# Optimization experiments

Measured on AMD Instinct MI355X. Metric: run time of the kernel, lower is better.

The kernel has to match this reference:

```python
import jax, jax.numpy as jnp
import numpy as np

N_NODES = 10000
N_EDGES = 160000
D = 256
P = 2.0  # exponent in |h_i - h_j|**p


def setup_inputs() -> dict:
    key = jax.random.key(0)
    k1, k2, k3, k4 = jax.random.split(key, 4)
    X = jax.random.normal(k1, (N_NODES, D), dtype=jnp.float32)
    edge_index = jax.random.randint(k2, (2, N_EDGES), 0, N_NODES, dtype=jnp.int64)
    # SAGEConv parameters (scaled like Glorot init)
    scale = 1.0 / np.sqrt(D)
    W_root = jax.random.normal(k3, (D, D), dtype=jnp.float32) * scale
    W_neigh = jax.random.normal(k4, (D, D), dtype=jnp.float32) * scale
    b = jnp.zeros((D,), dtype=jnp.float32)
    return {"X": X, "edge_index": edge_index, "W_root": W_root,
            "W_neigh": W_neigh, "b": b}


def reference(X, edge_index, W_root, W_neigh, b):
    n = X.shape[0]
    row, col = edge_index[0], edge_index[1]
    # degree of each target (row) node, used for both SAGE mean and scatter-mean
    ones = jnp.ones((row.shape[0],), dtype=X.dtype)
    deg = jax.ops.segment_sum(ones, row, num_segments=n)           # [N]
    denom = jnp.maximum(deg, 1.0)[:, None]                         # avoid 0-div
    # SAGEConv: h_i = W_root x_i + W_neigh mean_{j in N(i)} x_j + b
    neigh_sum = jax.ops.segment_sum(X[col], row, num_segments=n)   # [N, D]
    neigh_mean = neigh_sum / denom
    H = jax.nn.relu(X @ W_root + neigh_mean @ W_neigh + b)         # [N, D]
    # gather node diffs -> pow -> scatter-mean by row -> tanh
    diffs = jnp.abs(H[row] - H[col]) ** P                          # [E, D]
    gg = jax.ops.segment_sum(diffs, row, num_segments=n) / denom   # [N, D]
    return jnp.tanh(gg)
```

## Files before the change

### kernel.cpp

```cpp
#include <hip/hip_runtime.h>
#include <math.h>

#define N_NODES 10000
#define N_EDGES 160000
#define D 256
#define KDIM 512
#define CAP 64
#define SPLIT 5000

typedef short bf16x8 __attribute__((ext_vector_type(8)));
typedef float f32x4 __attribute__((ext_vector_type(4)));
typedef unsigned short u16x4 __attribute__((ext_vector_type(4)));
typedef unsigned short ushort_t;

__device__ __forceinline__ ushort_t f2bf(float f) {
    unsigned u = __builtin_bit_cast(unsigned, f);
    unsigned r = (u + 0x7fffu + ((u >> 16) & 1u)) >> 16;
    return (ushort_t)r;
}
__device__ __forceinline__ float bf2f(ushort_t u) {
    unsigned v = ((unsigned)u) << 16;
    return __builtin_bit_cast(float, v);
}

#define ZERO_BLOCKS 79
#define PREPW_BLOCKS 128
#define CASTX_BLOCKS 2500

__global__ void k_init(int* __restrict__ cursors,
                       const float* __restrict__ Wr, const float* __restrict__ Wn,
                       ushort_t* __restrict__ Wb,
                       const float* __restrict__ X, ushort_t* __restrict__ A) {
    __shared__ float tile[32][33];
    int b = blockIdx.x;
    int t = threadIdx.x;
    if (b < ZERO_BLOCKS) {
        int i = b * 256 + t;
        if (i < 2 * N_NODES) cursors[i] = 0;
    } else if (b < ZERO_BLOCKS + PREPW_BLOCKS) {
        int wb = b - ZERO_BLOCKS;
        int k0 = (wb & 15) * 32, n0 = (wb >> 4) * 32;
        {
            int r = t >> 3, c4 = t & 7;
            int k = k0 + r;
            const float* src = (k < D) ? (Wr + (size_t)k * D + n0 + c4 * 4)
                                       : (Wn + (size_t)(k - D) * D + n0 + c4 * 4);
            float4 v = *(const float4*)src;
            tile[r][c4 * 4 + 0] = v.x; tile[r][c4 * 4 + 1] = v.y;
            tile[r][c4 * 4 + 2] = v.z; tile[r][c4 * 4 + 3] = v.w;
        }
        __syncthreads();
        {
            int n = t >> 3, kq = t & 7;
            ushort4 o = make_ushort4(f2bf(tile[kq * 4 + 0][n]), f2bf(tile[kq * 4 + 1][n]),
                                     f2bf(tile[kq * 4 + 2][n]), f2bf(tile[kq * 4 + 3][n]));
            *(ushort4*)(Wb + (size_t)(n0 + n) * KDIM + k0 + kq * 4) = o;
        }
    } else {
        int nb = b - ZERO_BLOCKS - PREPW_BLOCKS;
        int node = nb * 4 + (t >> 6), lane = t & 63;
        if (node < N_NODES) {
            float4 v = *(const float4*)(X + (size_t)node * D + lane * 4);
            ushort4 o = make_ushort4(f2bf(v.x), f2bf(v.y), f2bf(v.z), f2bf(v.w));
            *(ushort4*)(A + (size_t)node * KDIM + lane * 4) = o;
        }
    }
}

__global__ void k_fill(const int* __restrict__ row, const int* __restrict__ col,
                       int* __restrict__ curLo, int* __restrict__ curHi,
                       int* __restrict__ csr_col, int e) {
    int i = blockIdx.x * blockDim.x + threadIdx.x;
    if (i < e) {
        int r = row[i], c = col[i];
        if (c < SPLIT) {
            int p = atomicAdd(&curLo[r], 1);
            csr_col[r * CAP + p] = c;
        } else {
            int p = atomicAdd(&curHi[r], 1);
            csr_col[r * CAP + CAP - 1 - p] = c;
        }
    }
}

__global__ void k_mean(const int* __restrict__ curLo, const int* __restrict__ curHi,
                       const int* __restrict__ csr_col, ushort_t* __restrict__ A) {
    int node = blockIdx.x * 4 + (threadIdx.x >> 6);
    int lane = threadIdx.x & 63;
    if (node >= N_NODES) return;
    int s0 = node * CAP;
    int nlo = curLo[node], nhi = curHi[node];
    float ax = 0.f, ay = 0.f, az = 0.f, aw = 0.f;
    #pragma unroll 1
    for (int half = 0; half < 2; ++half) {
        int s = half ? (s0 + CAP - nhi) : s0;
        int t = half ? (s0 + CAP) : (s0 + nlo);
        int e = s;
        for (; e + 8 <= t; e += 8) {
            int j0 = csr_col[e + 0], j1 = csr_col[e + 1], j2 = csr_col[e + 2], j3 = csr_col[e + 3];
            int j4 = csr_col[e + 4], j5 = csr_col[e + 5], j6 = csr_col[e + 6], j7 = csr_col[e + 7];
            ushort4 v0 = *(const ushort4*)(A + (size_t)j0 * KDIM + lane * 4);
            ushort4 v1 = *(const ushort4*)(A + (size_t)j1 * KDIM + lane * 4);
            ushort4 v2 = *(const ushort4*)(A + (size_t)j2 * KDIM + lane * 4);
            ushort4 v3 = *(const ushort4*)(A + (size_t)j3 * KDIM + lane * 4);
            ushort4 v4 = *(const ushort4*)(A + (size_t)j4 * KDIM + lane * 4);
            ushort4 v5 = *(const ushort4*)(A + (size_t)j5 * KDIM + lane * 4);
            ushort4 v6 = *(const ushort4*)(A + (size_t)j6 * KDIM + lane * 4);
            ushort4 v7 = *(const ushort4*)(A + (size_t)j7 * KDIM + lane * 4);
            ax += bf2f(v0.x) + bf2f(v1.x) + bf2f(v2.x) + bf2f(v3.x)
                + bf2f(v4.x) + bf2f(v5.x) + bf2f(v6.x) + bf2f(v7.x);
            ay += bf2f(v0.y) + bf2f(v1.y) + bf2f(v2.y) + bf2f(v3.y)
                + bf2f(v4.y) + bf2f(v5.y) + bf2f(v6.y) + bf2f(v7.y);
            az += bf2f(v0.z) + bf2f(v1.z) + bf2f(v2.z) + bf2f(v3.z)
                + bf2f(v4.z) + bf2f(v5.z) + bf2f(v6.z) + bf2f(v7.z);
            aw += bf2f(v0.w) + bf2f(v1.w) + bf2f(v2.w) + bf2f(v3.w)
                + bf2f(v4.w) + bf2f(v5.w) + bf2f(v6.w) + bf2f(v7.w);
        }
        for (; e < t; ++e) {
            int j = csr_col[e];
            ushort4 v = *(const ushort4*)(A + (size_t)j * KDIM + lane * 4);
            ax += bf2f(v.x); ay += bf2f(v.y); az += bf2f(v.z); aw += bf2f(v.w);
        }
    }
    int deg = nlo + nhi;
    float inv = 1.f / (float)(deg > 1 ? deg : 1);
    u16x4 o;
    o[0] = f2bf(ax * inv); o[1] = f2bf(ay * inv);
    o[2] = f2bf(az * inv); o[3] = f2bf(aw * inv);
    __builtin_nontemporal_store(o, (u16x4*)(A + (size_t)node * KDIM + D + lane * 4));
}

#define BM 64
#define BN 128
#define BK 32
#define LDK 40

__global__ __launch_bounds__(256) void k_gemm(
    const ushort_t* __restrict__ A, const ushort_t* __restrict__ Wb,
    const float* __restrict__ bias, ushort_t* __restrict__ H) {
    __shared__ ushort_t As[BM][LDK];
    __shared__ ushort_t Bs[BN][LDK];

    int tid = threadIdx.x;
    int lane = tid & 63;
    int wave = tid >> 6;
    int wm = wave >> 1;
    int wn = wave & 1;
    int row0 = blockIdx.x * BM;
    int col0 = blockIdx.y * BN;

    f32x4 acc[2][4];
    #pragma unroll
    for (int i = 0; i < 2; ++i)
        #pragma unroll
        for (int j = 0; j < 4; ++j)
            acc[i][j] = (f32x4){0.f, 0.f, 0.f, 0.f};

    int r_a = tid >> 2;
    int kq = tid & 3;

    for (int kk = 0; kk < KDIM; kk += BK) {
        int ga = row0 + r_a; if (ga >= N_NODES) ga = N_NODES - 1;
        ushort4 a0 = *(const ushort4*)(A + (size_t)ga * KDIM + kk + kq * 8);
        ushort4 a1 = *(const ushort4*)(A + (size_t)ga * KDIM + kk + kq * 8 + 4);
        ushort4 b0 = *(const ushort4*)(Wb + (size_t)(col0 + r_a) * KDIM + kk + kq * 8);
        ushort4 b1 = *(const ushort4*)(Wb + (size_t)(col0 + r_a) * KDIM + kk + kq * 8 + 4);
        ushort4 b2 = *(const ushort4*)(Wb + (size_t)(col0 + r_a + 64) * KDIM + kk + kq * 8);
        ushort4 b3 = *(const ushort4*)(Wb + (size_t)(col0 + r_a + 64) * KDIM + kk + kq * 8 + 4);

        __syncthreads();
        *(ushort4*)&As[r_a][kq * 8]          = a0;
        *(ushort4*)&As[r_a][kq * 8 + 4]      = a1;
        *(ushort4*)&Bs[r_a][kq * 8]          = b0;
        *(ushort4*)&Bs[r_a][kq * 8 + 4]      = b1;
        *(ushort4*)&Bs[r_a + 64][kq * 8]     = b2;
        *(ushort4*)&Bs[r_a + 64][kq * 8 + 4] = b3;
        __syncthreads();

        int fr = lane & 15, fg = (lane >> 4) * 8;
        bf16x8 aF[2], bF[4];
        #pragma unroll
        for (int mf = 0; mf < 2; ++mf)
            aF[mf] = *(const bf16x8*)&As[wm * 32 + mf * 16 + fr][fg];
        #pragma unroll
        for (int nf = 0; nf < 4; ++nf)
            bF[nf] = *(const bf16x8*)&Bs[wn * 64 + nf * 16 + fr][fg];
        #pragma unroll
        for (int mf = 0; mf < 2; ++mf)
            #pragma unroll
            for (int nf = 0; nf < 4; ++nf)
                acc[mf][nf] = __builtin_amdgcn_mfma_f32_16x16x32_bf16(
                    aF[mf], bF[nf], acc[mf][nf], 0, 0, 0);
    }

    int fc = lane & 15, frow = (lane >> 4) * 4;
    #pragma unroll
    for (int nf = 0; nf < 4; ++nf) {
        int c = col0 + wn * 64 + nf * 16 + fc;
        float bc = bias[c];
        #pragma unroll
        for (int mf = 0; mf < 2; ++mf) {
            #pragma unroll
            for (int q = 0; q < 4; ++q) {
                int r = row0 + wm * 32 + mf * 16 + frow + q;
                if (r < N_NODES) {
                    float h = acc[mf][nf][q] + bc;
                    H[(size_t)r * D + c] = f2bf(h > 0.f ? h : 0.f);
                }
            }
        }
    }
}

__global__ void k_out(const ushort_t* __restrict__ H,
                      const int* __restrict__ curLo, const int* __restrict__ curHi,
                      const int* __restrict__ csr_col,
                      float* __restrict__ out) {
    int node = blockIdx.x * 4 + (threadIdx.x >> 6);
    int lane = threadIdx.x & 63;
    if (node >= N_NODES) return;
    ushort4 hb = *(const ushort4*)(H + (size_t)node * D + lane * 4);
    float hx = bf2f(hb.x), hy = bf2f(hb.y), hz = bf2f(hb.z), hw = bf2f(hb.w);
    int s0 = node * CAP;
    int nlo = curLo[node], nhi = curHi[node];
    float ax = 0.f, ay = 0.f, az = 0.f, aw = 0.f;
    #pragma unroll 1
    for (int half = 0; half < 2; ++half) {
        int s = half ? (s0 + CAP - nhi) : s0;
        int t = half ? (s0 + CAP) : (s0 + nlo);
        int e = s;
        for (; e + 8 <= t; e += 8) {
            int j0 = csr_col[e + 0], j1 = csr_col[e + 1], j2 = csr_col[e + 2], j3 = csr_col[e + 3];
            int j4 = csr_col[e + 4], j5 = csr_col[e + 5], j6 = csr_col[e + 6], j7 = csr_col[e + 7];
            ushort4 v0 = *(const ushort4*)(H + (size_t)j0 * D + lane * 4);
            ushort4 v1 = *(const ushort4*)(H + (size_t)j1 * D + lane * 4);
            ushort4 v2 = *(const ushort4*)(H + (size_t)j2 * D + lane * 4);
            ushort4 v3 = *(const ushort4*)(H + (size_t)j3 * D + lane * 4);
            ushort4 v4 = *(const ushort4*)(H + (size_t)j4 * D + lane * 4);
            ushort4 v5 = *(const ushort4*)(H + (size_t)j5 * D + lane * 4);
            ushort4 v6 = *(const ushort4*)(H + (size_t)j6 * D + lane * 4);
            ushort4 v7 = *(const ushort4*)(H + (size_t)j7 * D + lane * 4);
            float d;
            d = hx - bf2f(v0.x); ax += d * d;  d = hy - bf2f(v0.y); ay += d * d;
            d = hz - bf2f(v0.z); az += d * d;  d = hw - bf2f(v0.w); aw += d * d;
            d = hx - bf2f(v1.x); ax += d * d;  d = hy - bf2f(v1.y); ay += d * d;
            d = hz - bf2f(v1.z); az += d * d;  d = hw - bf2f(v1.w); aw += d * d;
            d = hx - bf2f(v2.x); ax += d * d;  d = hy - bf2f(v2.y); ay += d * d;
            d = hz - bf2f(v2.z); az += d * d;  d = hw - bf2f(v2.w); aw += d * d;
            d = hx - bf2f(v3.x); ax += d * d;  d = hy - bf2f(v3.y); ay += d * d;
            d = hz - bf2f(v3.z); az += d * d;  d = hw - bf2f(v3.w); aw += d * d;
            d = hx - bf2f(v4.x); ax += d * d;  d = hy - bf2f(v4.y); ay += d * d;
            d = hz - bf2f(v4.z); az += d * d;  d = hw - bf2f(v4.w); aw += d * d;
            d = hx - bf2f(v5.x); ax += d * d;  d = hy - bf2f(v5.y); ay += d * d;
            d = hz - bf2f(v5.z); az += d * d;  d = hw - bf2f(v5.w); aw += d * d;
            d = hx - bf2f(v6.x); ax += d * d;  d = hy - bf2f(v6.y); ay += d * d;
            d = hz - bf2f(v6.z); az += d * d;  d = hw - bf2f(v6.w); aw += d * d;
            d = hx - bf2f(v7.x); ax += d * d;  d = hy - bf2f(v7.y); ay += d * d;
            d = hz - bf2f(v7.z); az += d * d;  d = hw - bf2f(v7.w); aw += d * d;
        }
        for (; e < t; ++e) {
            int j = csr_col[e];
            ushort4 v = *(const ushort4*)(H + (size_t)j * D + lane * 4);
            float d;
            d = hx - bf2f(v.x); ax += d * d;  d = hy - bf2f(v.y); ay += d * d;
            d = hz - bf2f(v.z); az += d * d;  d = hw - bf2f(v.w); aw += d * d;
        }
    }
    int deg = nlo + nhi;
    float inv = 1.f / (float)(deg > 1 ? deg : 1);
    f32x4 o;
    o[0] = tanhf(ax * inv); o[1] = tanhf(ay * inv);
    o[2] = tanhf(az * inv); o[3] = tanhf(aw * inv);
    __builtin_nontemporal_store(o, (f32x4*)(out + (size_t)node * D + lane * 4));
}


extern "C" void kernel_launch(void* const* d_in, const int* in_sizes, int n_in,
                              void* d_out, int out_size, void* d_ws, size_t ws_size,
                              hipStream_t stream) {
    const float* X    = (const float*)d_in[0];
    const int*   edge = (const int*)d_in[1];
    const float* Wr   = (const float*)d_in[2];
    const float* Wn   = (const float*)d_in[3];
    const float* bias = (const float*)d_in[4];
    float* out = (float*)d_out;

    char* ws = (char*)d_ws;
    size_t off = 0;
    auto alloc = [&](size_t bytes) -> void* {
        void* p = ws + off;
        off += (bytes + 255) & ~(size_t)255;
        return p;
    };
    int*      cursors = (int*)alloc(sizeof(int) * 2 * N_NODES);
    int*      csr_col = (int*)alloc(sizeof(int) * N_NODES * CAP);
    ushort_t* A       = (ushort_t*)alloc(sizeof(ushort_t) * (size_t)N_NODES * KDIM);
    ushort_t* Wb      = (ushort_t*)alloc(sizeof(ushort_t) * (size_t)D * KDIM);
    ushort_t* H       = (ushort_t*)alloc(sizeof(ushort_t) * (size_t)N_NODES * D);

    int* curLo = cursors;
    int* curHi = cursors + N_NODES;
    const int* row = edge;
    const int* col = edge + N_EDGES;

    k_init<<<ZERO_BLOCKS + PREPW_BLOCKS + CASTX_BLOCKS, 256, 0, stream>>>(
        cursors, Wr, Wn, Wb, X, A);
    k_fill<<<(N_EDGES + 255) / 256, 256, 0, stream>>>(row, col, curLo, curHi,
                                                      csr_col, N_EDGES);
    k_mean<<<2500, 256, 0, stream>>>(curLo, curHi, csr_col, A);

    dim3 ggrid((N_NODES + BM - 1) / BM, D / BN);
    k_gemm<<<ggrid, 256, 0, stream>>>(A, Wb, bias, H);

    k_out<<<2500, 256, 0, stream>>>(H, curLo, curHi, csr_col, out);
}
```

Measured before the change: 67.58 us.

## Split feature dimension into halves so gathers fit in cache

The gather kernels (mean aggregation and the output diff-pow-scatter) now run as two passes, each over a separate contiguous 128-column half of X and H. Each half-table is about 2.5 MB, so the random neighbour gathers should hit better in the L2/LLC. The low/high column-split CSR scheme is replaced by a single per-row cursor. The cost is two extra kernel launches, csr_col being read twice, narrower per-lane loads (ushort2 instead of ushort4), and extra writes of the Xlo/Xhi copies during init.

```diff
diff --git a/kernel.cpp b/kernel.cpp
--- a/kernel.cpp
+++ b/kernel.cpp
@@ -4,13 +4,14 @@
 #define N_NODES 10000
 #define N_EDGES 160000
 #define D 256
+#define HD 128
 #define KDIM 512
 #define CAP 64
-#define SPLIT 5000
 
 typedef short bf16x8 __attribute__((ext_vector_type(8)));
 typedef float f32x4 __attribute__((ext_vector_type(4)));
-typedef unsigned short u16x4 __attribute__((ext_vector_type(4)));
+typedef float f32x2 __attribute__((ext_vector_type(2)));
+typedef unsigned short u16x2 __attribute__((ext_vector_type(2)));
 typedef unsigned short ushort_t;
 
 __device__ __forceinline__ ushort_t f2bf(float f) {
@@ -23,20 +24,21 @@
     return __builtin_bit_cast(float, v);
 }
 
-#define ZERO_BLOCKS 79
+#define ZERO_BLOCKS 40
 #define PREPW_BLOCKS 128
 #define CASTX_BLOCKS 2500
 
-__global__ void k_init(int* __restrict__ cursors,
+__global__ void k_init(int* __restrict__ cursor,
                        const float* __restrict__ Wr, const float* __restrict__ Wn,
                        ushort_t* __restrict__ Wb,
-                       const float* __restrict__ X, ushort_t* __restrict__ A) {
+                       const float* __restrict__ X, ushort_t* __restrict__ A,
+                       ushort_t* __restrict__ Xlo, ushort_t* __restrict__ Xhi) {
     __shared__ float tile[32][33];
     int b = blockIdx.x;
     int t = threadIdx.x;
     if (b < ZERO_BLOCKS) {
         int i = b * 256 + t;
-        if (i < 2 * N_NODES) cursors[i] = 0;
+        if (i < N_NODES) cursor[i] = 0;
     } else if (b < ZERO_BLOCKS + PREPW_BLOCKS) {
         int wb = b - ZERO_BLOCKS;
         int k0 = (wb & 15) * 32, n0 = (wb >> 4) * 32;
@@ -63,71 +65,59 @@
             float4 v = *(const float4*)(X + (size_t)node * D + lane * 4);
             ushort4 o = make_ushort4(f2bf(v.x), f2bf(v.y), f2bf(v.z), f2bf(v.w));
             *(ushort4*)(A + (size_t)node * KDIM + lane * 4) = o;
+            if (lane < 32)
+                *(ushort4*)(Xlo + (size_t)node * HD + lane * 4) = o;
+            else
+                *(ushort4*)(Xhi + (size_t)node * HD + lane * 4 - HD) = o;
         }
     }
 }
 
 __global__ void k_fill(const int* __restrict__ row, const int* __restrict__ col,
-                       int* __restrict__ curLo, int* __restrict__ curHi,
-                       int* __restrict__ csr_col, int e) {
+                       int* __restrict__ cursor, int* __restrict__ csr_col, int e) {
     int i = blockIdx.x * blockDim.x + threadIdx.x;
     if (i < e) {
-        int r = row[i], c = col[i];
-        if (c < SPLIT) {
-            int p = atomicAdd(&curLo[r], 1);
-            csr_col[r * CAP + p] = c;
-        } else {
-            int p = atomicAdd(&curHi[r], 1);
-            csr_col[r * CAP + CAP - 1 - p] = c;
-        }
-    }
-}
-
-__global__ void k_mean(const int* __restrict__ curLo, const int* __restrict__ curHi,
-                       const int* __restrict__ csr_col, ushort_t* __restrict__ A) {
+        int r = row[i];
+        int p = atomicAdd(&cursor[r], 1);
+        csr_col[r * CAP + p] = col[i];
+    }
+}
+
+__global__ void k_mean(const int* __restrict__ cursor, const int* __restrict__ csr_col,
+                       const ushort_t* __restrict__ Xh, ushort_t* __restrict__ A, int h) {
     int node = blockIdx.x * 4 + (threadIdx.x >> 6);
     int lane = threadIdx.x & 63;
     if (node >= N_NODES) return;
-    int s0 = node * CAP;
-    int nlo = curLo[node], nhi = curHi[node];
-    float ax = 0.f, ay = 0.f, az = 0.f, aw = 0.f;
-    #pragma unroll 1
-    for (int half = 0; half < 2; ++half) {
-        int s = half ? (s0 + CAP - nhi) : s0;
-        int t = half ? (s0 + CAP) : (s0 + nlo);
-        int e = s;
-        for (; e + 8 <= t; e += 8) {
-            int j0 = csr_col[e + 0], j1 = csr_col[e + 1], j2 = csr_col[e + 2], j3 = csr_col[e + 3];
-            int j4 = csr_col[e + 4], j5 = csr_col[e + 5], j6 = csr_col[e + 6], j7 = csr_col[e + 7];
-            ushort4 v0 = *(const ushort4*)(A + (size_t)j0 * KDIM + lane * 4);
-            ushort4 v1 = *(const ushort4*)(A + (size_t)j1 * KDIM + lane * 4);
-            ushort4 v2 = *(const ushort4*)(A + (size_t)j2 * KDIM + lane * 4);
-            ushort4 v3 = *(const ushort4*)(A + (size_t)j3 * KDIM + lane * 4);
-            ushort4 v4 = *(const ushort4*)(A + (size_t)j4 * KDIM + lane * 4);
-            ushort4 v5 = *(const ushort4*)(A + (size_t)j5 * KDIM + lane * 4);
-            ushort4 v6 = *(const ushort4*)(A + (size_t)j6 * KDIM + lane * 4);
-            ushort4 v7 = *(const ushort4*)(A + (size_t)j7 * KDIM + lane * 4);
-            ax += bf2f(v0.x) + bf2f(v1.x) + bf2f(v2.x) + bf2f(v3.x)
-                + bf2f(v4.x) + bf2f(v5.x) + bf2f(v6.x) + bf2f(v7.x);
-            ay += bf2f(v0.y) + bf2f(v1.y) + bf2f(v2.y) + bf2f(v3.y)
-                + bf2f(v4.y) + bf2f(v5.y) + bf2f(v6.y) + bf2f(v7.y);
-            az += bf2f(v0.z) + bf2f(v1.z) + bf2f(v2.z) + bf2f(v3.z)
-                + bf2f(v4.z) + bf2f(v5.z) + bf2f(v6.z) + bf2f(v7.z);
-            aw += bf2f(v0.w) + bf2f(v1.w) + bf2f(v2.w) + bf2f(v3.w)
-                + bf2f(v4.w) + bf2f(v5.w) + bf2f(v6.w) + bf2f(v7.w);
-        }
-        for (; e < t; ++e) {
-            int j = csr_col[e];
-            ushort4 v = *(const ushort4*)(A + (size_t)j * KDIM + lane * 4);
-            ax += bf2f(v.x); ay += bf2f(v.y); az += bf2f(v.z); aw += bf2f(v.w);
-        }
-    }
-    int deg = nlo + nhi;
+    int dbase = lane * 2;
+    int deg = cursor[node];
+    int s0 = node * CAP, t1 = s0 + deg;
+    float ax = 0.f, ay = 0.f;
+    int e = s0;
+    for (; e + 8 <= t1; e += 8) {
+        int j0 = csr_col[e + 0], j1 = csr_col[e + 1], j2 = csr_col[e + 2], j3 = csr_col[e + 3];
+        int j4 = csr_col[e + 4], j5 = csr_col[e + 5], j6 = csr_col[e + 6], j7 = csr_col[e + 7];
+        ushort2 v0 = *(const ushort2*)(Xh + (size_t)j0 * HD + dbase);
+        ushort2 v1 = *(const ushort2*)(Xh + (size_t)j1 * HD + dbase);
+        ushort2 v2 = *(const ushort2*)(Xh + (size_t)j2 * HD + dbase);
+        ushort2 v3 = *(const ushort2*)(Xh + (size_t)j3 * HD + dbase);
+        ushort2 v4 = *(const ushort2*)(Xh + (size_t)j4 * HD + dbase);
+        ushort2 v5 = *(const ushort2*)(Xh + (size_t)j5 * HD + dbase);
+        ushort2 v6 = *(const ushort2*)(Xh + (size_t)j6 * HD + dbase);
+        ushort2 v7 = *(const ushort2*)(Xh + (size_t)j7 * HD + dbase);
+        ax += bf2f(v0.x) + bf2f(v1.x) + bf2f(v2.x) + bf2f(v3.x)
+            + bf2f(v4.x) + bf2f(v5.x) + bf2f(v6.x) + bf2f(v7.x);
+        ay += bf2f(v0.y) + bf2f(v1.y) + bf2f(v2.y) + bf2f(v3.y)
+            + bf2f(v4.y) + bf2f(v5.y) + bf2f(v6.y) + bf2f(v7.y);
+    }
+    for (; e < t1; ++e) {
+        int j = csr_col[e];
+        ushort2 v = *(const ushort2*)(Xh + (size_t)j * HD + dbase);
+        ax += bf2f(v.x); ay += bf2f(v.y);
+    }
     float inv = 1.f / (float)(deg > 1 ? deg : 1);
-    u16x4 o;
+    u16x2 o;
     o[0] = f2bf(ax * inv); o[1] = f2bf(ay * inv);
-    o[2] = f2bf(az * inv); o[3] = f2bf(aw * inv);
-    __builtin_nontemporal_store(o, (u16x4*)(A + (size_t)node * KDIM + D + lane * 4));
+    __builtin_nontemporal_store(o, (u16x2*)(A + (size_t)node * KDIM + D + h * HD + dbase));
 }
 
 #define BM 64
@@ -137,7 +127,8 @@
 
 __global__ __launch_bounds__(256) void k_gemm(
     const ushort_t* __restrict__ A, const ushort_t* __restrict__ Wb,
-    const float* __restrict__ bias, ushort_t* __restrict__ H) {
+    const float* __restrict__ bias,
+    ushort_t* __restrict__ Hlo, ushort_t* __restrict__ Hhi) {
     __shared__ ushort_t As[BM][LDK];
     __shared__ ushort_t Bs[BN][LDK];
 
@@ -193,10 +184,12 @@
                     aF[mf], bF[nf], acc[mf][nf], 0, 0, 0);
     }
 
+    ushort_t* Hh = (col0 < HD) ? Hlo : Hhi;
     int fc = lane & 15, frow = (lane >> 4) * 4;
     #pragma unroll
     for (int nf = 0; nf < 4; ++nf) {
         int c = col0 + wn * 64 + nf * 16 + fc;
+        int ch = c & (HD - 1);
         float bc = bias[c];
         #pragma unroll
         for (int mf = 0; mf < 2; ++mf) {
@@ -205,73 +198,57 @@
                 int r = row0 + wm * 32 + mf * 16 + frow + q;
                 if (r < N_NODES) {
                     float h = acc[mf][nf][q] + bc;
-                    H[(size_t)r * D + c] = f2bf(h > 0.f ? h : 0.f);
+                    Hh[(size_t)r * HD + ch] = f2bf(h > 0.f ? h : 0.f);
                 }
             }
         }
     }
 }
 
-__global__ void k_out(const ushort_t* __restrict__ H,
-                      const int* __restrict__ curLo, const int* __restrict__ curHi,
-                      const int* __restrict__ csr_col,
-                      float* __restrict__ out) {
+__global__ void k_out(const ushort_t* __restrict__ Hh,
+                      const int* __restrict__ cursor, const int* __restrict__ csr_col,
+                      float* __restrict__ out, int h) {
     int node = blockIdx.x * 4 + (threadIdx.x >> 6);
     int lane = threadIdx.x & 63;
     if (node >= N_NODES) return;
-    ushort4 hb = *(const ushort4*)(H + (size_t)node * D + lane * 4);
-    float hx = bf2f(hb.x), hy = bf2f(hb.y), hz = bf2f(hb.z), hw = bf2f(hb.w);
-    int s0 = node * CAP;
-    int nlo = curLo[node], nhi = curHi[node];
-    float ax = 0.f, ay = 0.f, az = 0.f, aw = 0.f;
-    #pragma unroll 1
-    for (int half = 0; half < 2; ++half) {
-        int s = half ? (s0 + CAP - nhi) : s0;
-        int t = half ? (s0 + CAP) : (s0 + nlo);
-        int e = s;
-        for (; e + 8 <= t; e += 8) {
-            int j0 = csr_col[e + 0], j1 = csr_col[e + 1], j2 = csr_col[e + 2], j3 = csr_col[e + 3];
-            int j4 = csr_col[e + 4], j5 = csr_col[e + 5], j6 = csr_col[e + 6], j7 = csr_col[e + 7];
-            ushort4 v0 = *(const ushort4*)(H + (size_t)j0 * D + lane * 4);
-            ushort4 v1 = *(const ushort4*)(H + (size_t)j1 * D + lane * 4);
-            ushort4 v2 = *(const ushort4*)(H + (size_t)j2 * D + lane * 4);
-            ushort4 v3 = *(const ushort4*)(H + (size_t)j3 * D + lane * 4);
-            ushort4 v4 = *(const ushort4*)(H + (size_t)j4 * D + lane * 4);
-            ushort4 v5 = *(const ushort4*)(H + (size_t)j5 * D + lane * 4);
-            ushort4 v6 = *(const ushort4*)(H + (size_t)j6 * D + lane * 4);
-            ushort4 v7 = *(const ushort4*)(H + (size_t)j7 * D + lane * 4);
-            float d;
-            d = hx - bf2f(v0.x); ax += d * d;  d = hy - bf2f(v0.y); ay += d * d;
-            d = hz - bf2f(v0.z); az += d * d;  d = hw - bf2f(v0.w); aw += d * d;
-            d = hx - bf2f(v1.x); ax += d * d;  d = hy - bf2f(v1.y); ay += d * d;
-            d = hz - bf2f(v1.z); az += d * d;  d = hw - bf2f(v1.w); aw += d * d;
-            d = hx - bf2f(v2.x); ax += d * d;  d = hy - bf2f(v2.y); ay += d * d;
-            d = hz - bf2f(v2.z); az += d * d;  d = hw - bf2f(v2.w); aw += d * d;
-            d = hx - bf2f(v3.x); ax += d * d;  d = hy - bf2f(v3.y); ay += d * d;
-            d = hz - bf2f(v3.z); az += d * d;  d = hw - bf2f(v3.w); aw += d * d;
-            d = hx - bf2f(v4.x); ax += d * d;  d = hy - bf2f(v4.y); ay += d * d;
-            d = hz - bf2f(v4.z); az += d * d;  d = hw - bf2f(v4.w); aw += d * d;
-            d = hx - bf2f(v5.x); ax += d * d;  d = hy - bf2f(v5.y); ay += d * d;
-            d = hz - bf2f(v5.z); az += d * d;  d = hw - bf2f(v5.w); aw += d * d;
-            d = hx - bf2f(v6.x); ax += d * d;  d = hy - bf2f(v6.y); ay += d * d;
-            d = hz - bf2f(v6.z); az += d * d;  d = hw - bf2f(v6.w); aw += d * d;
-            d = hx - bf2f(v7.x); ax += d * d;  d = hy - bf2f(v7.y); ay += d * d;
-            d = hz - bf2f(v7.z); az += d * d;  d = hw - bf2f(v7.w); aw += d * d;
-        }
-        for (; e < t; ++e) {
-            int j = csr_col[e];
-            ushort4 v = *(const ushort4*)(H + (size_t)j * D + lane * 4);
-            float d;
-            d = hx - bf2f(v.x); ax += d * d;  d = hy - bf2f(v.y); ay += d * d;
-            d = hz - bf2f(v.z); az += d * d;  d = hw - bf2f(v.w); aw += d * d;
-        }
-    }
-    int deg = nlo + nhi;
+    int dbase = lane * 2;
+    ushort2 hb = *(const ushort2*)(Hh + (size_t)node * HD + dbase);
+    float hx = bf2f(hb.x), hy = bf2f(hb.y);
+    int deg = cursor[node];
+    int s0 = node * CAP, t1 = s0 + deg;
+    float ax = 0.f, ay = 0.f;
+    int e = s0;
+    for (; e + 8 <= t1; e += 8) {
+        int j0 = csr_col[e + 0], j1 = csr_col[e + 1], j2 = csr_col[e + 2], j3 = csr_col[e + 3];
+        int j4 = csr_col[e + 4], j5 = csr_col[e + 5], j6 = csr_col[e + 6], j7 = csr_col[e + 7];
+        ushort2 v0 = *(const ushort2*)(Hh + (size_t)j0 * HD + dbase);
+        ushort2 v1 = *(const ushort2*)(Hh + (size_t)j1 * HD + dbase);
+        ushort2 v2 = *(const ushort2*)(Hh + (size_t)j2 * HD + dbase);
+        ushort2 v3 = *(const ushort2*)(Hh + (size_t)j3 * HD + dbase);
+        ushort2 v4 = *(const ushort2*)(Hh + (size_t)j4 * HD + dbase);
+        ushort2 v5 = *(const ushort2*)(Hh + (size_t)j5 * HD + dbase);
+        ushort2 v6 = *(const ushort2*)(Hh + (size_t)j6 * HD + dbase);
+        ushort2 v7 = *(const ushort2*)(Hh + (size_t)j7 * HD + dbase);
+        float d;
+        d = hx - bf2f(v0.x); ax += d * d;  d = hy - bf2f(v0.y); ay += d * d;
+        d = hx - bf2f(v1.x); ax += d * d;  d = hy - bf2f(v1.y); ay += d * d;
+        d = hx - bf2f(v2.x); ax += d * d;  d = hy - bf2f(v2.y); ay += d * d;
+        d = hx - bf2f(v3.x); ax += d * d;  d = hy - bf2f(v3.y); ay += d * d;
+        d = hx - bf2f(v4.x); ax += d * d;  d = hy - bf2f(v4.y); ay += d * d;
+        d = hx - bf2f(v5.x); ax += d * d;  d = hy - bf2f(v5.y); ay += d * d;
+        d = hx - bf2f(v6.x); ax += d * d;  d = hy - bf2f(v6.y); ay += d * d;
+        d = hx - bf2f(v7.x); ax += d * d;  d = hy - bf2f(v7.y); ay += d * d;
+    }
+    for (; e < t1; ++e) {
+        int j = csr_col[e];
+        ushort2 v = *(const ushort2*)(Hh + (size_t)j * HD + dbase);
+        float d;
+        d = hx - bf2f(v.x); ax += d * d;  d = hy - bf2f(v.y); ay += d * d;
+    }
     float inv = 1.f / (float)(deg > 1 ? deg : 1);
-    f32x4 o;
+    f32x2 o;
     o[0] = tanhf(ax * inv); o[1] = tanhf(ay * inv);
-    o[2] = tanhf(az * inv); o[3] = tanhf(aw * inv);
-    __builtin_nontemporal_store(o, (f32x4*)(out + (size_t)node * D + lane * 4));
+    __builtin_nontemporal_store(o, (f32x2*)(out + (size_t)node * D + h * HD + dbase));
 }
 
 
@@ -292,25 +269,27 @@
         off += (bytes + 255) & ~(size_t)255;
         return p;
     };
-    int*      cursors = (int*)alloc(sizeof(int) * 2 * N_NODES);
+    int*      cursor  = (int*)alloc(sizeof(int) * N_NODES);
     int*      csr_col = (int*)alloc(sizeof(int) * N_NODES * CAP);
     ushort_t* A       = (ushort_t*)alloc(sizeof(ushort_t) * (size_t)N_NODES * KDIM);
     ushort_t* Wb      = (ushort_t*)alloc(sizeof(ushort_t) * (size_t)D * KDIM);
-    ushort_t* H       = (ushort_t*)alloc(sizeof(ushort_t) * (size_t)N_NODES * D);
-
-    int* curLo = cursors;
-    int* curHi = cursors + N_NODES;
+    ushort_t* Xlo     = (ushort_t*)alloc(sizeof(ushort_t) * (size_t)N_NODES * HD);
+    ushort_t* Xhi     = (ushort_t*)alloc(sizeof(ushort_t) * (size_t)N_NODES * HD);
+    ushort_t* Hlo     = (ushort_t*)alloc(sizeof(ushort_t) * (size_t)N_NODES * HD);
+    ushort_t* Hhi     = (ushort_t*)alloc(sizeof(ushort_t) * (size_t)N_NODES * HD);
+
     const int* row = edge;
     const int* col = edge + N_EDGES;
 
     k_init<<<ZERO_BLOCKS + PREPW_BLOCKS + CASTX_BLOCKS, 256, 0, stream>>>(
-        cursors, Wr, Wn, Wb, X, A);
-    k_fill<<<(N_EDGES + 255) / 256, 256, 0, stream>>>(row, col, curLo, curHi,
-                                                      csr_col, N_EDGES);
-    k_mean<<<2500, 256, 0, stream>>>(curLo, curHi, csr_col, A);
+        cursor, Wr, Wn, Wb, X, A, Xlo, Xhi);
+    k_fill<<<(N_EDGES + 255) / 256, 256, 0, stream>>>(row, col, cursor, csr_col, N_EDGES);
+    k_mean<<<2500, 256, 0, stream>>>(cursor, csr_col, Xlo, A, 0);
+    k_mean<<<2500, 256, 0, stream>>>(cursor, csr_col, Xhi, A, 1);
 
     dim3 ggrid((N_NODES + BM - 1) / BM, D / BN);
-    k_gemm<<<ggrid, 256, 0, stream>>>(A, Wb, bias, H);
-
-    k_out<<<2500, 256, 0, stream>>>(H, curLo, curHi, csr_col, out);
-}
+    k_gemm<<<ggrid, 256, 0, stream>>>(A, Wb, bias, Hlo, Hhi);
+
+    k_out<<<2500, 256, 0, stream>>>(Hlo, cursor, csr_col, out, 0);
+    k_out<<<2500, 256, 0, stream>>>(Hhi, cursor, csr_col, out, 1);
+}
```

Measured after the change: 76.77 us. +13.6%, slower.
